# Optimization experiments

Measured on AMD Instinct MI355X. Metric: run time of the kernel, lower is better.

The kernel has to match this reference:

```python
import jax, jax.numpy as jnp
import numpy as np
import math

B, S, D, H = 4, 2048, 1024, 16
DH = D // H  # dim per head = 64


def setup_inputs() -> dict:
    key = jax.random.key(0)
    ks = jax.random.split(key, 12)
    scale = 0.02
    inp = {
        "query": jax.random.normal(ks[0], (B, S, D), jnp.float32),
        "key": jax.random.normal(ks[1], (B, S, D), jnp.float32),
        "value": jax.random.normal(ks[2], (B, S, D), jnp.float32),
        "mask": jnp.zeros((B, S), jnp.float32),  # additive mask, 0 = attend
        "Wq": jax.random.normal(ks[3], (D, D), jnp.float32) * scale,
        "bq": jnp.zeros((D,), jnp.float32),
        "Wk": jax.random.normal(ks[4], (D, D), jnp.float32) * scale,
        "bk": jnp.zeros((D,), jnp.float32),
        "Wv": jax.random.normal(ks[5], (D, D), jnp.float32) * scale,
        "bv": jnp.zeros((D,), jnp.float32),
        "Wo": jax.random.normal(ks[6], (D, D), jnp.float32) * scale,
        "bo": jnp.zeros((D,), jnp.float32),
    }
    return inp


def reference(query, key, value, mask, Wq, bq, Wk, bk, Wv, bv, Wo, bo):
    # Linear projections (torch Linear: x @ W.T + b; here W stored as (in, out))
    def shape(x):  # (B,S,D) -> (B,H,S,DH)
        return x.reshape(B, S, H, DH).transpose(0, 2, 1, 3)

    q = shape(query @ Wq + bq) / math.sqrt(DH)
    k = shape(key @ Wk + bk)
    v = shape(value @ Wv + bv)

    # scores: (B,H,S,S)
    scores = jnp.einsum("bhqd,bhkd->bhqk", q, k)
    scores = scores + mask[:, None, None, :]  # additive mask broadcast
    weights = jax.nn.softmax(scores, axis=-1)
    # dropout omitted (eval mode / p effectively 0 for reference)
    context = jnp.einsum("bhqk,bhkd->bhqd", weights, v)
    context = context.transpose(0, 2, 1, 3).reshape(B, S, D)
    out = context @ Wo + bo
    return out
```

## Files before the change

kernel.cpp:

```cpp
#include <hip/hip_runtime.h>
#include <hip/hip_bf16.h>

#define B_  4
#define S_  2048
#define D_  1024
#define H_  16
#define DH_ 64
#define M_  (B_*S_)

typedef __attribute__((ext_vector_type(8)))  short    bf16x8;
typedef __attribute__((ext_vector_type(4)))  float    f32x4;
typedef __attribute__((ext_vector_type(16))) float    f32x16;
typedef __attribute__((ext_vector_type(2)))  unsigned u32x2;

#define LOG2E 1.4426950408889634f

__device__ __forceinline__ void g2l16(const void* g, void* l) {
    __builtin_amdgcn_global_load_lds(
        (const __attribute__((address_space(1))) unsigned*)g,
        (__attribute__((address_space(3))) unsigned*)l, 16, 0, 0);
}

__global__ __launch_bounds__(256) void wtrans4(
    const float* __restrict__ W0, const float* __restrict__ W1,
    const float* __restrict__ W2, const float* __restrict__ W3,
    __hip_bfloat16* __restrict__ T0, __hip_bfloat16* __restrict__ T1,
    __hip_bfloat16* __restrict__ T2, __hip_bfloat16* __restrict__ T3)
{
    const float* W = blockIdx.z == 0 ? W0 : (blockIdx.z == 1 ? W1 : (blockIdx.z == 2 ? W2 : W3));
    __hip_bfloat16* Wt = blockIdx.z == 0 ? T0 : (blockIdx.z == 1 ? T1 : (blockIdx.z == 2 ? T2 : T3));
    __shared__ float t[32][33];
    const int bx = blockIdx.x * 32;
    const int by = blockIdx.y * 32;
    const int tx = threadIdx.x, ty = threadIdx.y;
    #pragma unroll
    for (int i = 0; i < 32; i += 8)
        t[ty + i][tx] = W[(size_t)(by + ty + i) * D_ + bx + tx];
    __syncthreads();
    #pragma unroll
    for (int i = 0; i < 32; i += 8)
        Wt[(size_t)(bx + ty + i) * D_ + by + tx] = __float2bfloat16(t[tx][ty + i]);
}

__global__ __launch_bounds__(256, 3) void gemm_qkv(
    const float* __restrict__ Xq, const float* __restrict__ Xk, const float* __restrict__ Xv,
    const __hip_bfloat16* __restrict__ WtQ, const __hip_bfloat16* __restrict__ WtK,
    const __hip_bfloat16* __restrict__ WtV,
    const float* __restrict__ bq, const float* __restrict__ bk, const float* __restrict__ bv,
    __hip_bfloat16* __restrict__ Yq, __hip_bfloat16* __restrict__ Yk,
    __hip_bfloat16* __restrict__ Yv)
{
    __shared__ char Ab[16384];
    __shared__ char Bb[16384];

    const int flat = blockIdx.x;
    const int xcd  = flat & 7;
    const int t    = flat >> 3;
    const int bz   = t >> 6;
    const int r    = t & 63;
    const int m0   = (xcd * 8 + (r >> 3)) * 128;
    const int n0   = (r & 7) * 128;

    const float* X = bz == 0 ? Xq : (bz == 1 ? Xk : Xv);
    const __hip_bfloat16* Wt = bz == 0 ? WtQ : (bz == 1 ? WtK : WtV);
    const float* bias = bz == 0 ? bq : (bz == 1 ? bk : bv);
    __hip_bfloat16* Y = bz == 0 ? Yq : (bz == 1 ? Yk : Yv);
    const float scale = bz == 0 ? 0.125f * LOG2E : 1.0f;

    const int tid = threadIdx.x;
    const int w = tid >> 6, l = tid & 63;
    const int wm = w >> 1, wn = w & 1;
    const int li = l & 15, lg = l >> 4;

    f32x4 acc[4][4];
    #pragma unroll
    for (int a = 0; a < 4; ++a)
        #pragma unroll
        for (int b = 0; b < 4; ++b)
            acc[a][b] = (f32x4){0.f, 0.f, 0.f, 0.f};

    for (int k0 = 0; k0 < D_; k0 += 64) {
        #pragma unroll
        for (int p = 0; p < 4; ++p) {
            int sl = p * 256 + tid;
            int row = sl >> 3, s = sl & 7;
            g2l16(Wt + (size_t)(n0 + row) * D_ + k0 + s * 8, Bb + sl * 16);
        }
        #pragma unroll
        for (int p = 0; p < 8; ++p) {
            int idx = p * 256 + tid;
            int row = idx >> 4, c4 = idx & 15;
            float4 xa = *(const float4*)(X + (size_t)(m0 + row) * D_ + k0 + c4 * 4);
            union { __hip_bfloat16 h[4]; u32x2 u; } cv;
            cv.h[0] = __float2bfloat16(xa.x); cv.h[1] = __float2bfloat16(xa.y);
            cv.h[2] = __float2bfloat16(xa.z); cv.h[3] = __float2bfloat16(xa.w);
            *(u32x2*)(Ab + row * 128 + c4 * 8) = cv.u;
        }
        asm volatile("s_waitcnt vmcnt(0)");
        __syncthreads();

        #pragma unroll
        for (int kh = 0; kh < 2; ++kh) {
            bf16x8 af[4], bfr[4];
            #pragma unroll
            for (int mt = 0; mt < 4; ++mt)
                af[mt] = *(const bf16x8*)(Ab + (wm * 64 + mt * 16 + li) * 128 + kh * 64 + lg * 16);
            #pragma unroll
            for (int nt = 0; nt < 4; ++nt)
                bfr[nt] = *(const bf16x8*)(Bb + (wn * 64 + nt * 16 + li) * 128 + kh * 64 + lg * 16);
            #pragma unroll
            for (int mt = 0; mt < 4; ++mt)
                #pragma unroll
                for (int nt = 0; nt < 4; ++nt)
                    acc[mt][nt] = __builtin_amdgcn_mfma_f32_16x16x32_bf16(
                        af[mt], bfr[nt], acc[mt][nt], 0, 0, 0);
        }
        __syncthreads();
    }

    #pragma unroll
    for (int mt = 0; mt < 4; ++mt) {
        #pragma unroll
        for (int nt = 0; nt < 4; ++nt) {
            int col = n0 + wn * 64 + nt * 16 + li;
            float bv_ = bias[col];
            #pragma unroll
            for (int i = 0; i < 4; ++i) {
                int row = m0 + wm * 64 + mt * 16 + lg * 4 + i;
                float v = (acc[mt][nt][i] + bv_) * scale;
                if (bz == 2) {
                    int b = row >> 11, s = row & (S_ - 1);
                    int h = col >> 6,  dh = col & 63;
                    Y[((((size_t)b * H_ + h) * DH_ + dh) << 11) + s] = __float2bfloat16(v);
                } else {
                    Y[(size_t)row * D_ + col] = __float2bfloat16(v);
                }
            }
        }
    }
}

__global__ __launch_bounds__(256, 3) void gemm_out(
    const __hip_bfloat16* __restrict__ X, const __hip_bfloat16* __restrict__ Wt,
    const float* __restrict__ bias, float* __restrict__ Y)
{
    __shared__ char Ab[16384];
    __shared__ char Bb[16384];

    const int flat = blockIdx.x;
    const int xcd  = flat & 7;
    const int t    = flat >> 3;
    const int m0   = (xcd * 8 + (t >> 3)) * 128;
    const int n0   = (t & 7) * 128;

    const int tid = threadIdx.x;
    const int w = tid >> 6, l = tid & 63;
    const int wm = w >> 1, wn = w & 1;
    const int li = l & 15, lg = l >> 4;

    f32x4 acc[4][4];
    #pragma unroll
    for (int a = 0; a < 4; ++a)
        #pragma unroll
        for (int b = 0; b < 4; ++b)
            acc[a][b] = (f32x4){0.f, 0.f, 0.f, 0.f};

    for (int k0 = 0; k0 < D_; k0 += 64) {
        #pragma unroll
        for (int p = 0; p < 4; ++p) {
            int sl = p * 256 + tid;
            int row = sl >> 3, s = sl & 7;
            g2l16(X  + (size_t)(m0 + row) * D_ + k0 + s * 8, Ab + sl * 16);
            g2l16(Wt + (size_t)(n0 + row) * D_ + k0 + s * 8, Bb + sl * 16);
        }
        asm volatile("s_waitcnt vmcnt(0)");
        __syncthreads();

        #pragma unroll
        for (int kh = 0; kh < 2; ++kh) {
            bf16x8 af[4], bfr[4];
            #pragma unroll
            for (int mt = 0; mt < 4; ++mt)
                af[mt] = *(const bf16x8*)(Ab + (wm * 64 + mt * 16 + li) * 128 + kh * 64 + lg * 16);
            #pragma unroll
            for (int nt = 0; nt < 4; ++nt)
                bfr[nt] = *(const bf16x8*)(Bb + (wn * 64 + nt * 16 + li) * 128 + kh * 64 + lg * 16);
            #pragma unroll
            for (int mt = 0; mt < 4; ++mt)
                #pragma unroll
                for (int nt = 0; nt < 4; ++nt)
                    acc[mt][nt] = __builtin_amdgcn_mfma_f32_16x16x32_bf16(
                        af[mt], bfr[nt], acc[mt][nt], 0, 0, 0);
        }
        __syncthreads();
    }

    #pragma unroll
    for (int mt = 0; mt < 4; ++mt) {
        #pragma unroll
        for (int nt = 0; nt < 4; ++nt) {
            int col = n0 + wn * 64 + nt * 16 + li;
            float bv_ = bias[col];
            #pragma unroll
            for (int i = 0; i < 4; ++i) {
                int row = m0 + wm * 64 + mt * 16 + lg * 4 + i;
                Y[(size_t)row * D_ + col] = acc[mt][nt][i] + bv_;
            }
        }
    }
}

__global__ __launch_bounds__(256, 4) void attn_mfma(
    const __hip_bfloat16* __restrict__ q, const __hip_bfloat16* __restrict__ k,
    const __hip_bfloat16* __restrict__ vt, const float* __restrict__ mask,
    __hip_bfloat16* __restrict__ ctx)
{
    __shared__ char Kb[2][8192];
    __shared__ char Vb[2][8192];
    __shared__ float mlds[S_];

    const int tid = threadIdx.x;
    const int w = tid >> 6, l = tid & 63;
    const int q31 = l & 31, hi = l >> 5;

    const int bid = blockIdx.x;
    const int j = bid >> 3;
    const int bh = (bid & 7) * 8 + (j >> 4);
    const int q0 = (j & 15) * 128;
    const int bb = bh >> 4, hh = bh & 15;

    const __hip_bfloat16* kbase = k  + (size_t)bb * S_ * D_ + hh * 64;
    const __hip_bfloat16* vbase = vt + (size_t)bh * (DH_ * S_);

    for (int i = tid; i < S_ / 4; i += 256) {
        float4 mv = ((const float4*)(mask + (size_t)bb * S_))[i];
        mv.x *= LOG2E; mv.y *= LOG2E; mv.z *= LOG2E; mv.w *= LOG2E;
        ((float4*)mlds)[i] = mv;
    }

    const int qrow = q0 + w * 32 + q31;
    const __hip_bfloat16* qp = q + (size_t)(bb * S_ + qrow) * D_ + hh * 64;
    bf16x8 qf[4];
    #pragma unroll
    for (int mf = 0; mf < 4; ++mf)
        qf[mf] = *(const bf16x8*)(qp + mf * 16 + hi * 8);

    f32x16 ot0, ot1;
    #pragma unroll
    for (int r = 0; r < 16; ++r) { ot0[r] = 0.f; ot1[r] = 0.f; }
    float mrun = -1e30f, lsum = 0.f;

    #pragma unroll
    for (int c = 0; c < 2; ++c) {
        int sl = c * 256 + tid, row = sl >> 3, s = sl & 7, sw = s ^ (row & 7);
        g2l16(kbase + (size_t)row * D_ + sw * 8, Kb[0] + sl * 16);
        g2l16(vbase + (size_t)row * S_ + sw * 8, Vb[0] + sl * 16);
    }
    asm volatile("s_waitcnt vmcnt(0)");
    __syncthreads();

    int cur = 0;
    for (int kt = 0; kt < S_; kt += 64) {
        if (kt + 64 < S_) {
            #pragma unroll
            for (int c = 0; c < 2; ++c) {
                int sl = c * 256 + tid, row = sl >> 3, s = sl & 7, sw = s ^ (row & 7);
                g2l16(kbase + (size_t)(kt + 64 + row) * D_ + sw * 8, Kb[cur ^ 1] + sl * 16);
                g2l16(vbase + (size_t)row * S_ + (kt + 64) + sw * 8, Vb[cur ^ 1] + sl * 16);
            }
        }

        #pragma unroll
        for (int ks = 0; ks < 2; ++ks) {
            f32x16 sc;
            #pragma unroll
            for (int g = 0; g < 4; ++g) {
                f32x4 mq = *(const f32x4*)(mlds + kt + ks * 32 + g * 8 + hi * 4);
                sc[g * 4 + 0] = mq[0]; sc[g * 4 + 1] = mq[1];
                sc[g * 4 + 2] = mq[2]; sc[g * 4 + 3] = mq[3];
            }
            const int arow = ks * 32 + q31;
            __builtin_amdgcn_s_setprio(1);
            #pragma unroll
            for (int mf = 0; mf < 4; ++mf) {
                int slot = (mf * 2 + hi) ^ (arow & 7);
                bf16x8 kf = *(const bf16x8*)(Kb[cur] + arow * 128 + slot * 16);
                sc = __builtin_amdgcn_mfma_f32_32x32x16_bf16(kf, qf[mf], sc, 0, 0, 0);
            }
            __builtin_amdgcn_s_setprio(0);
            float t0 = fmaxf(fmaxf(sc[0], sc[1]), sc[2]);
            float t1 = fmaxf(fmaxf(sc[3], sc[4]), sc[5]);
            float t2 = fmaxf(fmaxf(sc[6], sc[7]), sc[8]);
            float t3 = fmaxf(fmaxf(sc[9], sc[10]), sc[11]);
            float t4 = fmaxf(fmaxf(sc[12], sc[13]), sc[14]);
            float mt = fmaxf(fmaxf(fmaxf(t0, t1), t2), fmaxf(fmaxf(t3, t4), sc[15]));
            if (!__all(mt <= mrun + 8.0f)) {
                float mo = fmaxf(mt, __shfl_xor(mt, 32));
                float mnew = fmaxf(mrun, mo);
                float al = __builtin_amdgcn_exp2f(mrun - mnew);
                lsum *= al;
                #pragma unroll
                for (int r = 0; r < 16; ++r) { ot0[r] *= al; ot1[r] *= al; }
                mrun = mnew;
            }
            float ps[4] = {0.f, 0.f, 0.f, 0.f};
            #pragma unroll
            for (int r = 0; r < 16; ++r) {
                float e = __builtin_amdgcn_exp2f(sc[r] - mrun);
                sc[r] = e;
                ps[r & 3] += e;
            }
            lsum += (ps[0] + ps[1]) + (ps[2] + ps[3]);

            unsigned pw[8];
            #pragma unroll
            for (int m = 0; m < 8; ++m) {
                float lo = sc[2 * m], hp = sc[2 * m + 1];
                unsigned r_;
                asm("v_cvt_pk_bf16_f32 %0, %1, %2" : "=v"(r_) : "v"(lo), "v"(hp));
                pw[m] = r_;
            }
            u32x2 s02 = __builtin_amdgcn_permlane32_swap(pw[0], pw[2], false, false);
            u32x2 s13 = __builtin_amdgcn_permlane32_swap(pw[1], pw[3], false, false);
            u32x2 s46 = __builtin_amdgcn_permlane32_swap(pw[4], pw[6], false, false);
            u32x2 s57 = __builtin_amdgcn_permlane32_swap(pw[5], pw[7], false, false);
            union { unsigned u[4]; bf16x8 v; } pf0, pf1;
            pf0.u[0] = s02[0]; pf0.u[1] = s13[0]; pf0.u[2] = s02[1]; pf0.u[3] = s13[1];
            pf1.u[0] = s46[0]; pf1.u[1] = s57[0]; pf1.u[2] = s46[1]; pf1.u[3] = s57[1];

            __builtin_amdgcn_s_setprio(1);
            #pragma unroll
            for (int kh = 0; kh < 2; ++kh) {
                bf16x8 pf = kh ? pf1.v : pf0.v;
                #pragma unroll
                for (int dt = 0; dt < 2; ++dt) {
                    int row = dt * 32 + q31;
                    int slot = (ks * 4 + kh * 2 + hi) ^ (row & 7);
                    bf16x8 vf = *(const bf16x8*)(Vb[cur] + row * 128 + slot * 16);
                    if (dt == 0)
                        ot0 = __builtin_amdgcn_mfma_f32_32x32x16_bf16(vf, pf, ot0, 0, 0, 0);
                    else
                        ot1 = __builtin_amdgcn_mfma_f32_32x32x16_bf16(vf, pf, ot1, 0, 0, 0);
                }
            }
            __builtin_amdgcn_s_setprio(0);
        }
        asm volatile("s_waitcnt vmcnt(0)");
        __syncthreads();
        cur ^= 1;
    }

    float lt = lsum + __shfl_xor(lsum, 32);
    float inv = 1.0f / lt;
    __hip_bfloat16* cp = ctx + (size_t)(bb * S_ + qrow) * D_ + hh * 64;
    #pragma unroll
    for (int dt = 0; dt < 2; ++dt) {
        #pragma unroll
        for (int g = 0; g < 4; ++g) {
            float v0 = (dt ? ot1[g * 4 + 0] : ot0[g * 4 + 0]) * inv;
            float v1 = (dt ? ot1[g * 4 + 1] : ot0[g * 4 + 1]) * inv;
            float v2 = (dt ? ot1[g * 4 + 2] : ot0[g * 4 + 2]) * inv;
            float v3 = (dt ? ot1[g * 4 + 3] : ot0[g * 4 + 3]) * inv;
            unsigned w0, w1;
            asm("v_cvt_pk_bf16_f32 %0, %1, %2" : "=v"(w0) : "v"(v0), "v"(v1));
            asm("v_cvt_pk_bf16_f32 %0, %1, %2" : "=v"(w1) : "v"(v2), "v"(v3));
            u32x2 st; st[0] = w0; st[1] = w1;
            *(u32x2*)(cp + dt * 32 + g * 8 + hi * 4) = st;
        }
    }
}

extern "C" void kernel_launch(void* const* d_in, const int* in_sizes, int n_in,
                              void* d_out, int out_size, void* d_ws, size_t ws_size,
                              hipStream_t stream) {
    const float* query = (const float*)d_in[0];
    const float* key_  = (const float*)d_in[1];
    const float* value = (const float*)d_in[2];
    const float* mask  = (const float*)d_in[3];
    const float* Wq = (const float*)d_in[4];
    const float* bq = (const float*)d_in[5];
    const float* Wk = (const float*)d_in[6];
    const float* bk = (const float*)d_in[7];
    const float* Wv = (const float*)d_in[8];
    const float* bv = (const float*)d_in[9];
    const float* Wo = (const float*)d_in[10];
    const float* bo = (const float*)d_in[11];
    float* out = (float*)d_out;

    const size_t WSZ = (size_t)D_ * D_;
    const size_t ASZ = (size_t)M_ * D_;
    __hip_bfloat16* p   = (__hip_bfloat16*)d_ws;
    __hip_bfloat16* WtQ = p;            p += WSZ;
    __hip_bfloat16* WtK = p;            p += WSZ;
    __hip_bfloat16* WtV = p;            p += WSZ;
    __hip_bfloat16* WtO = p;            p += WSZ;
    __hip_bfloat16* qb  = p;            p += ASZ;
    __hip_bfloat16* kb  = p;            p += ASZ;
    __hip_bfloat16* vtb = p;            p += ASZ;
    __hip_bfloat16* cb  = p;            p += ASZ;

    wtrans4<<<dim3(32, 32, 4), dim3(32, 8), 0, stream>>>(Wq, Wk, Wv, Wo, WtQ, WtK, WtV, WtO);

    gemm_qkv<<<dim3(1536), 256, 0, stream>>>(
        query, key_, value, WtQ, WtK, WtV, bq, bk, bv, qb, kb, vtb);

    attn_mfma<<<dim3((S_ / 128) * B_ * H_), 256, 0, stream>>>(qb, kb, vtb, mask, cb);

    gemm_out<<<dim3(512), 256, 0, stream>>>(cb, WtO, bo, out);
}
```

Baseline: 221.0 us.

## Double-buffer LDS tiles in projection GEMMs to overlap loads with MFMA

Both the QKV and output projection GEMMs now use two LDS buffers. The next K-tile is issued (global_load_lds for bf16, register float4 loads for the fp32 activations) before the MFMAs on the current tile run, and only then waited on. This hides global-memory latency behind compute and drops one barrier per iteration. In exchange it doubles LDS use to 64KB per block, lowers launch bounds occupancy from 3 to 2, and raises register pressure from holding eight float4 prefetch values.

```diff
diff --git a/kernel.cpp b/kernel.cpp
--- a/kernel.cpp
+++ b/kernel.cpp
@@ -42,7 +42,7 @@
         Wt[(size_t)(bx + ty + i) * D_ + by + tx] = __float2bfloat16(t[tx][ty + i]);
 }
 
-__global__ __launch_bounds__(256, 3) void gemm_qkv(
+__global__ __launch_bounds__(256, 2) void gemm_qkv(
     const float* __restrict__ Xq, const float* __restrict__ Xk, const float* __restrict__ Xv,
     const __hip_bfloat16* __restrict__ WtQ, const __hip_bfloat16* __restrict__ WtK,
     const __hip_bfloat16* __restrict__ WtV,
@@ -50,8 +50,8 @@
     __hip_bfloat16* __restrict__ Yq, __hip_bfloat16* __restrict__ Yk,
     __hip_bfloat16* __restrict__ Yv)
 {
-    __shared__ char Ab[16384];
-    __shared__ char Bb[16384];
+    __shared__ char Ab[2][16384];
+    __shared__ char Bb[2][16384];
 
     const int flat = blockIdx.x;
     const int xcd  = flat & 7;
@@ -72,6 +72,9 @@
     const int wm = w >> 1, wn = w & 1;
     const int li = l & 15, lg = l >> 4;
 
+    const int arow = tid >> 4, ac4 = tid & 15;
+    const int brow = tid >> 3, bs = tid & 7;
+
     f32x4 acc[4][4];
     #pragma unroll
     for (int a = 0; a < 4; ++a)
@@ -79,35 +82,57 @@
         for (int b = 0; b < 4; ++b)
             acc[a][b] = (f32x4){0.f, 0.f, 0.f, 0.f};
 
+    {
+        #pragma unroll
+        for (int p = 0; p < 4; ++p) {
+            int sl = p * 256 + tid, row = sl >> 3, s = sl & 7;
+            g2l16(Wt + (size_t)(n0 + row) * D_ + s * 8, Bb[0] + sl * 16);
+        }
+        float4 xa[8];
+        #pragma unroll
+        for (int p = 0; p < 8; ++p) {
+            int idx = p * 256 + tid, row = idx >> 4, c4 = idx & 15;
+            xa[p] = *(const float4*)(X + (size_t)(m0 + row) * D_ + c4 * 4);
+        }
+        asm volatile("s_waitcnt vmcnt(0)");
+        #pragma unroll
+        for (int p = 0; p < 8; ++p) {
+            int idx = p * 256 + tid, row = idx >> 4, c4 = idx & 15;
+            union { __hip_bfloat16 h[4]; u32x2 u; } cv;
+            cv.h[0] = __float2bfloat16(xa[p].x); cv.h[1] = __float2bfloat16(xa[p].y);
+            cv.h[2] = __float2bfloat16(xa[p].z); cv.h[3] = __float2bfloat16(xa[p].w);
+            *(u32x2*)(Ab[0] + row * 128 + c4 * 8) = cv.u;
+        }
+    }
+    __syncthreads();
+
+    int cur = 0;
     for (int k0 = 0; k0 < D_; k0 += 64) {
-        #pragma unroll
-        for (int p = 0; p < 4; ++p) {
-            int sl = p * 256 + tid;
-            int row = sl >> 3, s = sl & 7;
-            g2l16(Wt + (size_t)(n0 + row) * D_ + k0 + s * 8, Bb + sl * 16);
-        }
-        #pragma unroll
-        for (int p = 0; p < 8; ++p) {
-            int idx = p * 256 + tid;
-            int row = idx >> 4, c4 = idx & 15;
-            float4 xa = *(const float4*)(X + (size_t)(m0 + row) * D_ + k0 + c4 * 4);
-            union { __hip_bfloat16 h[4]; u32x2 u; } cv;
-            cv.h[0] = __float2bfloat16(xa.x); cv.h[1] = __float2bfloat16(xa.y);
-            cv.h[2] = __float2bfloat16(xa.z); cv.h[3] = __float2bfloat16(xa.w);
-            *(u32x2*)(Ab + row * 128 + c4 * 8) = cv.u;
-        }
-        asm volatile("s_waitcnt vmcnt(0)");
-        __syncthreads();
+        const int kn = k0 + 64;
+        const bool pref = kn < D_;
+        float4 xa[8];
+        if (pref) {
+            #pragma unroll
+            for (int p = 0; p < 4; ++p) {
+                int sl = p * 256 + tid, row = sl >> 3, s = sl & 7;
+                g2l16(Wt + (size_t)(n0 + row) * D_ + kn + s * 8, Bb[cur ^ 1] + sl * 16);
+            }
+            #pragma unroll
+            for (int p = 0; p < 8; ++p) {
+                int idx = p * 256 + tid, row = idx >> 4, c4 = idx & 15;
+                xa[p] = *(const float4*)(X + (size_t)(m0 + row) * D_ + kn + c4 * 4);
+            }
+        }
 
         #pragma unroll
         for (int kh = 0; kh < 2; ++kh) {
             bf16x8 af[4], bfr[4];
             #pragma unroll
             for (int mt = 0; mt < 4; ++mt)
-                af[mt] = *(const bf16x8*)(Ab + (wm * 64 + mt * 16 + li) * 128 + kh * 64 + lg * 16);
+                af[mt] = *(const bf16x8*)(Ab[cur] + (wm * 64 + mt * 16 + li) * 128 + kh * 64 + lg * 16);
             #pragma unroll
             for (int nt = 0; nt < 4; ++nt)
-                bfr[nt] = *(const bf16x8*)(Bb + (wn * 64 + nt * 16 + li) * 128 + kh * 64 + lg * 16);
+                bfr[nt] = *(const bf16x8*)(Bb[cur] + (wn * 64 + nt * 16 + li) * 128 + kh * 64 + lg * 16);
             #pragma unroll
             for (int mt = 0; mt < 4; ++mt)
                 #pragma unroll
@@ -115,7 +140,20 @@
                     acc[mt][nt] = __builtin_amdgcn_mfma_f32_16x16x32_bf16(
                         af[mt], bfr[nt], acc[mt][nt], 0, 0, 0);
         }
+
+        if (pref) {
+            asm volatile("s_waitcnt vmcnt(0)");
+            #pragma unroll
+            for (int p = 0; p < 8; ++p) {
+                int idx = p * 256 + tid, row = idx >> 4, c4 = idx & 15;
+                union { __hip_bfloat16 h[4]; u32x2 u; } cv;
+                cv.h[0] = __float2bfloat16(xa[p].x); cv.h[1] = __float2bfloat16(xa[p].y);
+                cv.h[2] = __float2bfloat16(xa[p].z); cv.h[3] = __float2bfloat16(xa[p].w);
+                *(u32x2*)(Ab[cur ^ 1] + row * 128 + c4 * 8) = cv.u;
+            }
+        }
         __syncthreads();
+        cur ^= 1;
     }
 
     #pragma unroll
@@ -138,14 +176,15 @@
             }
         }
     }
-}
-
-__global__ __launch_bounds__(256, 3) void gemm_out(
+    (void)arow; (void)ac4; (void)brow; (void)bs;
+}
+
+__global__ __launch_bounds__(256, 2) void gemm_out(
     const __hip_bfloat16* __restrict__ X, const __hip_bfloat16* __restrict__ Wt,
     const float* __restrict__ bias, float* __restrict__ Y)
 {
-    __shared__ char Ab[16384];
-    __shared__ char Bb[16384];
+    __shared__ char Ab[2][16384];
+    __shared__ char Bb[2][16384];
 
     const int flat = blockIdx.x;
     const int xcd  = flat & 7;
@@ -165,26 +204,36 @@
         for (int b = 0; b < 4; ++b)
             acc[a][b] = (f32x4){0.f, 0.f, 0.f, 0.f};
 
+    #pragma unroll
+    for (int p = 0; p < 4; ++p) {
+        int sl = p * 256 + tid, row = sl >> 3, s = sl & 7;
+        g2l16(X  + (size_t)(m0 + row) * D_ + s * 8, Ab[0] + sl * 16);
+        g2l16(Wt + (size_t)(n0 + row) * D_ + s * 8, Bb[0] + sl * 16);
+    }
+    asm volatile("s_waitcnt vmcnt(0)");
+    __syncthreads();
+
+    int cur = 0;
     for (int k0 = 0; k0 < D_; k0 += 64) {
-        #pragma unroll
-        for (int p = 0; p < 4; ++p) {
-            int sl = p * 256 + tid;
-            int row = sl >> 3, s = sl & 7;
-            g2l16(X  + (size_t)(m0 + row) * D_ + k0 + s * 8, Ab + sl * 16);
-            g2l16(Wt + (size_t)(n0 + row) * D_ + k0 + s * 8, Bb + sl * 16);
-        }
-        asm volatile("s_waitcnt vmcnt(0)");
-        __syncthreads();
+        const int kn = k0 + 64;
+        if (kn < D_) {
+            #pragma unroll
+            for (int p = 0; p < 4; ++p) {
+                int sl = p * 256 + tid, row = sl >> 3, s = sl & 7;
+                g2l16(X  + (size_t)(m0 + row) * D_ + kn + s * 8, Ab[cur ^ 1] + sl * 16);
+                g2l16(Wt + (size_t)(n0 + row) * D_ + kn + s * 8, Bb[cur ^ 1] + sl * 16);
+            }
+        }
 
         #pragma unroll
         for (int kh = 0; kh < 2; ++kh) {
             bf16x8 af[4], bfr[4];
             #pragma unroll
             for (int mt = 0; mt < 4; ++mt)
-                af[mt] = *(const bf16x8*)(Ab + (wm * 64 + mt * 16 + li) * 128 + kh * 64 + lg * 16);
+                af[mt] = *(const bf16x8*)(Ab[cur] + (wm * 64 + mt * 16 + li) * 128 + kh * 64 + lg * 16);
             #pragma unroll
             for (int nt = 0; nt < 4; ++nt)
-                bfr[nt] = *(const bf16x8*)(Bb + (wn * 64 + nt * 16 + li) * 128 + kh * 64 + lg * 16);
+                bfr[nt] = *(const bf16x8*)(Bb[cur] + (wn * 64 + nt * 16 + li) * 128 + kh * 64 + lg * 16);
             #pragma unroll
             for (int mt = 0; mt < 4; ++mt)
                 #pragma unroll
@@ -192,7 +241,10 @@
                     acc[mt][nt] = __builtin_amdgcn_mfma_f32_16x16x32_bf16(
                         af[mt], bfr[nt], acc[mt][nt], 0, 0, 0);
         }
+
+        asm volatile("s_waitcnt vmcnt(0)");
         __syncthreads();
+        cur ^= 1;
     }
 
     #pragma unroll
```

Measured after the change: 247.6 us. +12.0%, slower.
